# Optimization experiments

Hardware: AMD Instinct MI355X
Metric: run time of the kernel (lower is better)

The kernel has to match this reference:

```python
import jax, jax.numpy as jnp
import numpy as np

N = 100000
E = 2000000
F = 64          # in_features == out_features (required by attention * h_j)
BETA = 0.5
NEG_SLOPE = 0.01  # torch F.leaky_relu default


def setup_inputs() -> dict:
    key = jax.random.key(0)
    k1, k2, k3, k4, k5, k6 = jax.random.split(key, 6)
    h = jax.random.normal(k1, (N, F), dtype=jnp.float32)
    adj = jax.random.randint(k2, (2, E), 0, N, dtype=jnp.int64)
    amount = jax.random.uniform(k3, (E,), dtype=jnp.float32)
    count = jax.random.uniform(k4, (E,), dtype=jnp.float32)
    fc_w = jax.random.normal(k5, (F, 2 * F), dtype=jnp.float32) * (1.0 / np.sqrt(2 * F))
    fc_b = jax.random.normal(k6, (F,), dtype=jnp.float32) * 0.01
    return {"h": h, "adj": adj, "amount": amount, "count": count,
            "fc_w": fc_w, "fc_b": fc_b}


def _minmax_norm(x):
    lo, hi = x.min(), x.max()
    return (x - lo) / (hi - lo + 1e-8)


def reference(h, adj, amount, count, fc_w, fc_b):
    # per-edge weight from normalized amount/count
    edge_weight = BETA * _minmax_norm(amount) + (1.0 - BETA) * _minmax_norm(count)  # [E]

    src, dst = adj[0], adj[1]
    h_i = h[src]                     # [E, F]
    h_j = h[dst]                     # [E, F]
    h_cat = jnp.concatenate([h_i, h_j], axis=1)  # [E, 2F]

    score = jnp.einsum('ef,of->eo', h_cat, fc_w) + fc_b  # [E, F_out]
    score = jnp.where(score >= 0, score, NEG_SLOPE * score)  # leaky_relu
    score = score * edge_weight[:, None]

    # softmax over ALL edges (dim 0), per feature, as in the original
    attention = jax.nn.softmax(score, axis=0)  # [E, F]

    agg = jnp.zeros_like(h).at[src].add(attention * h_j)  # scatter-add -> [N, F]
    return agg
```

## Files before the change

kernel.cpp:

```cpp
#include <hip/hip_runtime.h>
#include <hip/hip_fp16.h>
#include <math.h>

#define FDIM   64
#define NB     16
#define BSHIFT 7
#define BMASK  127
#define EPTA   16
#define CHUNKA (EPTA * 256)
#define SCH    1024
#define DMASK  0xFFFFF

__global__ __launch_bounds__(256) void count_mm_k(const int* __restrict__ src,
                                                  const float* __restrict__ amount,
                                                  const float* __restrict__ count,
                                                  int* __restrict__ mat,
                                                  float4* __restrict__ partial,
                                                  double* __restrict__ colsum,
                                                  int E, int nblkA, int nbkt) {
  __shared__ int lhist[1024];
  __shared__ float4 lred[4];
  for (int k = threadIdx.x; k < nbkt; k += 256) lhist[k] = 0;
  if (blockIdx.x == 0)
    for (int i = threadIdx.x; i < 1024; i += 256) colsum[i] = 0.0;
  __syncthreads();
  float amin = 3.4e38f, amax = -3.4e38f, cmin = 3.4e38f, cmax = -3.4e38f;
  int e0 = blockIdx.x * CHUNKA + threadIdx.x * EPTA;
  if (e0 + EPTA <= E) {
    #pragma unroll
    for (int q = 0; q < EPTA; q += 4) {
      int4   s4 = *(const int4*)(src + e0 + q);
      float4 a4 = *(const float4*)(amount + e0 + q);
      float4 c4 = *(const float4*)(count + e0 + q);
      atomicAdd(&lhist[s4.x >> BSHIFT], 1);
      atomicAdd(&lhist[s4.y >> BSHIFT], 1);
      atomicAdd(&lhist[s4.z >> BSHIFT], 1);
      atomicAdd(&lhist[s4.w >> BSHIFT], 1);
      amin = fminf(amin, fminf(fminf(a4.x, a4.y), fminf(a4.z, a4.w)));
      amax = fmaxf(amax, fmaxf(fmaxf(a4.x, a4.y), fmaxf(a4.z, a4.w)));
      cmin = fminf(cmin, fminf(fminf(c4.x, c4.y), fminf(c4.z, c4.w)));
      cmax = fmaxf(cmax, fmaxf(fmaxf(c4.x, c4.y), fmaxf(c4.z, c4.w)));
    }
  } else {
    for (int e = e0; e < E; e++) {
      atomicAdd(&lhist[src[e] >> BSHIFT], 1);
      float a = amount[e], c = count[e];
      amin = fminf(amin, a); amax = fmaxf(amax, a);
      cmin = fminf(cmin, c); cmax = fmaxf(cmax, c);
    }
  }
  #pragma unroll
  for (int off = 32; off; off >>= 1) {
    amin = fminf(amin, __shfl_down(amin, off));
    amax = fmaxf(amax, __shfl_down(amax, off));
    cmin = fminf(cmin, __shfl_down(cmin, off));
    cmax = fmaxf(cmax, __shfl_down(cmax, off));
  }
  if ((threadIdx.x & 63) == 0) lred[threadIdx.x >> 6] = make_float4(amin, amax, cmin, cmax);
  __syncthreads();
  for (int k = threadIdx.x; k < nbkt; k += 256)
    mat[(size_t)k * nblkA + blockIdx.x] = lhist[k];
  if (threadIdx.x == 0) {
    float4 r = lred[0];
    #pragma unroll
    for (int w = 1; w < 4; w++) {
      r.x = fminf(r.x, lred[w].x); r.y = fmaxf(r.y, lred[w].y);
      r.z = fminf(r.z, lred[w].z); r.w = fmaxf(r.w, lred[w].w);
    }
    partial[blockIdx.x] = r;
  }
}

__global__ __launch_bounds__(256) void scan1_k(const int* __restrict__ v,
                                               int* __restrict__ bsum, int M) {
  __shared__ int lds[256];
  int t = threadIdx.x, b = blockIdx.x;
  int s = 0;
  for (int i = b * SCH + t; i < min((b + 1) * SCH, M); i += 256) s += v[i];
  lds[t] = s; __syncthreads();
  for (int off = 128; off; off >>= 1) {
    if (t < off) lds[t] += lds[t + off];
    __syncthreads();
  }
  if (t == 0) bsum[b] = lds[0];
}

__global__ __launch_bounds__(256) void scan2_k(const int* __restrict__ bsum,
                                               int* __restrict__ bexcl, int nchunk,
                                               const float4* __restrict__ partial,
                                               float* __restrict__ mmf, int nb) {
  __shared__ int lds[256];
  int t = threadIdx.x;
  int running = 0;
  for (int c0 = 0; c0 < nchunk; c0 += 256) {
    int x = (c0 + t < nchunk) ? bsum[c0 + t] : 0;
    lds[t] = x; __syncthreads();
    for (int off = 1; off < 256; off <<= 1) {
      int v = (t >= off) ? lds[t - off] : 0;
      __syncthreads();
      lds[t] += v; __syncthreads();
    }
    if (c0 + t < nchunk) bexcl[c0 + t] = running + lds[t] - x;
    running += lds[255];
    __syncthreads();
  }
  float amin = 3.4e38f, amax = -3.4e38f, cmin = 3.4e38f, cmax = -3.4e38f;
  for (int i = t; i < nb; i += 256) {
    float4 p = partial[i];
    amin = fminf(amin, p.x); amax = fmaxf(amax, p.y);
    cmin = fminf(cmin, p.z); cmax = fmaxf(cmax, p.w);
  }
  #pragma unroll
  for (int off = 32; off; off >>= 1) {
    amin = fminf(amin, __shfl_down(amin, off));
    amax = fmaxf(amax, __shfl_down(amax, off));
    cmin = fminf(cmin, __shfl_down(cmin, off));
    cmax = fmaxf(cmax, __shfl_down(cmax, off));
  }
  __shared__ float4 lred[4];
  if ((t & 63) == 0) lred[t >> 6] = make_float4(amin, amax, cmin, cmax);
  __syncthreads();
  if (t == 0) {
    float4 r = lred[0];
    #pragma unroll
    for (int w = 1; w < 4; w++) {
      r.x = fminf(r.x, lred[w].x); r.y = fmaxf(r.y, lred[w].y);
      r.z = fminf(r.z, lred[w].z); r.w = fmaxf(r.w, lred[w].w);
    }
    mmf[0] = r.x; mmf[1] = r.y; mmf[2] = r.z; mmf[3] = r.w;
  }
}

__global__ __launch_bounds__(256) void scan3_k(const int* __restrict__ v,
                                               const int* __restrict__ bexcl,
                                               int* __restrict__ smat, int M) {
  __shared__ int lds[256];
  int t = threadIdx.x, b = blockIdx.x;
  int running = bexcl[b];
  for (int tile = 0; tile < SCH; tile += 256) {
    int i = b * SCH + tile + t;
    int x = (i < M) ? v[i] : 0;
    lds[t] = x; __syncthreads();
    for (int off = 1; off < 256; off <<= 1) {
      int vv = (t >= off) ? lds[t - off] : 0;
      __syncthreads();
      lds[t] += vv; __syncthreads();
    }
    if (i < M) smat[i] = running + lds[t] - x;
    running += lds[255];
    __syncthreads();
  }
}

__global__ __launch_bounds__(256) void scatter_k(const int* __restrict__ src,
                                                 const int* __restrict__ dst,
                                                 const float* __restrict__ amount,
                                                 const float* __restrict__ count,
                                                 const float* __restrict__ mmf,
                                                 const int* __restrict__ smat,
                                                 int2* __restrict__ payload,
                                                 int E, int nblkA, int nbkt) {
  __shared__ int cntb[1024];
  __shared__ int baseb[1024];
  __shared__ int sbase[1024];
  __shared__ int tmp[256];
  __shared__ int2 lpay[CHUNKA];
  __shared__ int lgpos[CHUNKA];
  const int t = threadIdx.x, blk = blockIdx.x;
  for (int k = t; k < nbkt; k += 256) {
    cntb[k] = 0;
    sbase[k] = smat[(size_t)k * nblkA + blk];
  }
  __syncthreads();
  const float amin = mmf[0], amax = mmf[1], cmin = mmf[2], cmax = mmf[3];
  const float L2E = 1.4426950408889634f;
  const float ascale = 0.5f * L2E / (amax - amin + 1e-8f);
  const float cscale = 0.5f * L2E / (cmax - cmin + 1e-8f);
  int e0 = blk * CHUNKA + t * EPTA;
  const bool full = (e0 + EPTA <= E);
  int4 S[4]; int4 D[4]; float4 A[4]; float4 C[4];
  if (full) {
    #pragma unroll
    for (int q = 0; q < 4; q++) {
      S[q] = *(const int4*)(src + e0 + 4 * q);
      D[q] = *(const int4*)(dst + e0 + 4 * q);
      A[q] = *(const float4*)(amount + e0 + 4 * q);
      C[q] = *(const float4*)(count + e0 + 4 * q);
      atomicAdd(&cntb[S[q].x >> BSHIFT], 1);
      atomicAdd(&cntb[S[q].y >> BSHIFT], 1);
      atomicAdd(&cntb[S[q].z >> BSHIFT], 1);
      atomicAdd(&cntb[S[q].w >> BSHIFT], 1);
    }
  } else {
    for (int e = e0; e < E; e++) atomicAdd(&cntb[src[e] >> BSHIFT], 1);
  }
  __syncthreads();
  int running = 0;
  for (int c0 = 0; c0 < nbkt; c0 += 256) {
    int x = (c0 + t < nbkt) ? cntb[c0 + t] : 0;
    tmp[t] = x; __syncthreads();
    for (int off = 1; off < 256; off <<= 1) {
      int v = (t >= off) ? tmp[t - off] : 0;
      __syncthreads();
      tmp[t] += v; __syncthreads();
    }
    if (c0 + t < nbkt) baseb[c0 + t] = running + tmp[t] - x;
    running += tmp[255];
    __syncthreads();
  }
  for (int k = t; k < nbkt; k += 256) cntb[k] = baseb[k];
  __syncthreads();
  auto ins = [&](int s, int d, float a, float c) {
    int b = s >> BSHIFT;
    float ew = (a - amin) * ascale + (c - cmin) * cscale;
    int pos = atomicAdd(&cntb[b], 1);
    lpay[pos] = make_int2(d | ((s & BMASK) << 20), __float_as_int(ew));
    lgpos[pos] = sbase[b] + (pos - baseb[b]);
  };
  if (full) {
    #pragma unroll
    for (int q = 0; q < 4; q++) {
      ins(S[q].x, D[q].x, A[q].x, C[q].x);
      ins(S[q].y, D[q].y, A[q].y, C[q].y);
      ins(S[q].z, D[q].z, A[q].z, C[q].z);
      ins(S[q].w, D[q].w, A[q].w, C[q].w);
    }
  } else {
    for (int e = e0; e < E; e++) ins(src[e], dst[e], amount[e], count[e]);
  }
  __syncthreads();
  const int ned = min(CHUNKA, E - blk * CHUNKA);
  for (int i = t; i < ned; i += 256) payload[lgpos[i]] = lpay[i];
}

__global__ __launch_bounds__(256) void binB_k(const int2* __restrict__ payload,
                                              const int* __restrict__ smat,
                                              int* __restrict__ hist,
                                              int* __restrict__ offsets,
                                              int2* __restrict__ edge_s,
                                              int E, int nblkA, int nbkt, int N) {
  __shared__ int fcnt[128];
  __shared__ int fs[128];
  __shared__ int fcur[128];
  const int b = blockIdx.x;
  const int t = threadIdx.x;
  const int base = smat[(size_t)b * nblkA];
  const int end  = (b + 1 < nbkt) ? smat[(size_t)(b + 1) * nblkA] : E;
  if (t < 128) fcnt[t] = 0;
  __syncthreads();
  for (int i = base + t; i < end; i += 256)
    atomicAdd(&fcnt[payload[i].x >> 20], 1);
  __syncthreads();
  if (t < 128) fs[t] = fcnt[t];
  __syncthreads();
  for (int off = 1; off < 128; off <<= 1) {
    int v = 0;
    if (t < 128 && t >= off) v = fs[t - off];
    __syncthreads();
    if (t < 128) fs[t] += v;
    __syncthreads();
  }
  if (t < 128) {
    int excl = fs[t] - fcnt[t];
    fcur[t] = base + excl;
    int node = (b << BSHIFT) + t;
    if (node < N) { hist[node] = fcnt[t]; offsets[node] = base + excl; }
  }
  __syncthreads();
  for (int i = base + t; i < end; i += 256) {
    int2 v = payload[i];
    int pos = atomicAdd(&fcur[v.x >> 20], 1);
    edge_s[pos] = make_int2(v.x & DMASK, v.y);
  }
}

__global__ __launch_bounds__(128) void pre_gemm(const float* __restrict__ h,
                                                const float* __restrict__ fc_w,
                                                const float* __restrict__ fc_b,
                                                float* __restrict__ G1,
                                                __half2* __restrict__ P, int N) {
  __shared__ float hs[NB * FDIM];
  const int t = threadIdx.x;
  const int o = t & 63, half = t >> 6;
  float w[FDIM];
  const float* wrow = fc_w + o * 128 + half * 64;
  #pragma unroll
  for (int f = 0; f < FDIM; f += 4) {
    float4 v = *(const float4*)(wrow + f);
    w[f] = v.x; w[f + 1] = v.y; w[f + 2] = v.z; w[f + 3] = v.w;
  }
  const float bias = (half == 0) ? fc_b[o] : 0.0f;
  const int n0 = blockIdx.x * NB;
  const int nrows = min(NB, N - n0);
  for (int i = t; i < nrows * FDIM; i += 128) hs[i] = h[(size_t)n0 * FDIM + i];
  __syncthreads();
  for (int n = 0; n < nrows; n++) {
    float acc = bias;
    #pragma unroll
    for (int f = 0; f < FDIM; f += 4) {
      float4 hv = *(const float4*)(&hs[n * FDIM + f]);
      acc += hv.x * w[f] + hv.y * w[f + 1] + hv.z * w[f + 2] + hv.w * w[f + 3];
    }
    if (half == 0) {
      G1[(size_t)(n0 + n) * FDIM + o] = acc;
    } else {
      P[(size_t)(n0 + n) * FDIM + o] =
          __halves2half2(__float2half(acc), __float2half(hs[n * FDIM + o]));
    }
  }
}

__device__ __forceinline__ float2 unpack_h2(unsigned u) {
  __half2 v = *(__half2*)&u;
  return make_float2(__low2float(v), __high2float(v));
}

__global__ __launch_bounds__(256) void fused_k(const int* __restrict__ offsets,
                                               const int* __restrict__ hist,
                                               const int2* __restrict__ edge_s,
                                               const float* __restrict__ G1,
                                               const unsigned* __restrict__ P,
                                               double* __restrict__ colsum,
                                               float* __restrict__ out, int N) {
  const int lane = threadIdx.x & 63;
  const int wid = blockIdx.x * 4 + (threadIdx.x >> 6);
  const int nw = gridDim.x * 4;
  float csum = 0.0f;
  for (int n = wid; n < N; n += nw) {
    float g1 = G1[(size_t)n * FDIM + lane];
    float acc = 0.0f;
    int start = offsets[n], cnt = hist[n];
    for (int j0 = 0; j0 < cnt; j0 += 64) {
      int m = min(64, cnt - j0);
      int2 p = make_int2(0, 0);
      if (lane < m) p = edge_s[start + j0 + lane];
      int j = 0;
      for (; j + 16 <= m; j += 16) {
        int dd[16]; float ee[16]; unsigned uu[16];
        #pragma unroll
        for (int k = 0; k < 16; k++) {
          dd[k] = __builtin_amdgcn_readlane(p.x, j + k);
          ee[k] = __int_as_float(__builtin_amdgcn_readlane(p.y, j + k));
        }
        #pragma unroll
        for (int k = 0; k < 16; k++) uu[k] = P[(size_t)dd[k] * FDIM + lane];
        #pragma unroll
        for (int k = 0; k < 16; k++) {
          float2 v = unpack_h2(uu[k]);
          float sc = g1 + v.x;
          sc = fmaxf(sc, 0.01f * sc);
          float x = exp2f(sc * ee[k]);
          csum += x;
          acc += x * v.y;
        }
      }
      for (; j < m; j += 8) {
        int rem = m - j;
        int dd[8]; float ee[8], wm[8]; unsigned uu[8];
        #pragma unroll
        for (int k = 0; k < 8; k++) {
          dd[k] = __builtin_amdgcn_readlane(p.x, j + k);
          ee[k] = __int_as_float(__builtin_amdgcn_readlane(p.y, j + k));
          wm[k] = (k < rem) ? 1.0f : 0.0f;
        }
        #pragma unroll
        for (int k = 0; k < 8; k++) uu[k] = P[(size_t)dd[k] * FDIM + lane];
        #pragma unroll
        for (int k = 0; k < 8; k++) {
          float2 v = unpack_h2(uu[k]);
          float sc = g1 + v.x;
          sc = fmaxf(sc, 0.01f * sc);
          float x = exp2f(sc * ee[k]) * wm[k];
          csum += x;
          acc += x * v.y;
        }
      }
    }
    out[(size_t)n * FDIM + lane] = acc;
  }
  __shared__ float part[256];
  part[threadIdx.x] = csum;
  __syncthreads();
  if (threadIdx.x < 64) {
    float tot = part[threadIdx.x] + part[threadIdx.x + 64] +
                part[threadIdx.x + 128] + part[threadIdx.x + 192];
    atomicAdd(&colsum[threadIdx.x * 16], (double)tot);
  }
}

__global__ __launch_bounds__(256) void scale_k(float4* __restrict__ out4,
                                               const double* __restrict__ colsum,
                                               int total4) {
  __shared__ float rinv_s[64];
  if (threadIdx.x < 64) rinv_s[threadIdx.x] = (float)(1.0 / colsum[threadIdx.x * 16]);
  __syncthreads();
  const float4* r4 = (const float4*)rinv_s;
  int idx = blockIdx.x * blockDim.x + threadIdx.x;
  int stride = gridDim.x * blockDim.x;
  for (int i = idx; i < total4; i += stride) {
    float4 v = out4[i];
    float4 r = r4[i & 15];
    v.x *= r.x; v.y *= r.y; v.z *= r.z; v.w *= r.w;
    out4[i] = v;
  }
}

extern "C" void kernel_launch(void* const* d_in, const int* in_sizes, int n_in,
                              void* d_out, int out_size, void* d_ws, size_t ws_size,
                              hipStream_t stream) {
  const float* h      = (const float*)d_in[0];
  const int*   adj    = (const int*)d_in[1];
  const float* amount = (const float*)d_in[2];
  const float* count  = (const float*)d_in[3];
  const float* fc_w   = (const float*)d_in[4];
  const float* fc_b   = (const float*)d_in[5];
  float* out = (float*)d_out;

  const int E = in_sizes[2];
  const int N = in_sizes[0] / FDIM;
  const int* src = adj;
  const int* dst = adj + E;
  const int nbkt  = (N + BMASK) >> BSHIFT;
  const int nblkA = (E + CHUNKA - 1) / CHUNKA;
  const int M = nbkt * nblkA;
  const int nchunk = (M + SCH - 1) / SCH;

  char* ws = (char*)d_ws;
  size_t off = 0;
  auto alloc = [&](size_t bytes) { void* p = ws + off; off += (bytes + 255) & ~(size_t)255; return p; };
  float*    G1      = (float*)alloc((size_t)N * FDIM * sizeof(float));
  __half2*  P       = (__half2*)alloc((size_t)N * FDIM * sizeof(__half2));
  int2*     edge_s  = (int2*)alloc((size_t)E * sizeof(int2));
  int2*     payload = (int2*)alloc((size_t)E * sizeof(int2));
  int*      hist    = (int*)alloc((size_t)N * sizeof(int));
  int*      offsets = (int*)alloc((size_t)N * sizeof(int));
  int*      mat     = (int*)alloc((size_t)M * sizeof(int));
  int*      smat    = (int*)alloc((size_t)M * sizeof(int));
  int*      bsum    = (int*)alloc((size_t)nchunk * sizeof(int));
  int*      bexcl   = (int*)alloc((size_t)nchunk * sizeof(int));
  float4*   mmpart  = (float4*)alloc((size_t)nblkA * sizeof(float4));
  double*   colsum  = (double*)alloc(1024 * sizeof(double));
  float*    mmf     = (float*)alloc(4 * sizeof(float));

  count_mm_k<<<nblkA, 256, 0, stream>>>(src, amount, count, mat, mmpart, colsum, E, nblkA, nbkt);
  scan1_k<<<nchunk, 256, 0, stream>>>(mat, bsum, M);
  scan2_k<<<1, 256, 0, stream>>>(bsum, bexcl, nchunk, mmpart, mmf, nblkA);
  scan3_k<<<nchunk, 256, 0, stream>>>(mat, bexcl, smat, M);
  scatter_k<<<nblkA, 256, 0, stream>>>(src, dst, amount, count, mmf, smat, payload, E, nblkA, nbkt);
  binB_k<<<nbkt, 256, 0, stream>>>(payload, smat, hist, offsets, edge_s, E, nblkA, nbkt, N);
  pre_gemm<<<(N + NB - 1) / NB, 128, 0, stream>>>(h, fc_w, fc_b, G1, P, N);
  fused_k<<<4096, 256, 0, stream>>>(offsets, hist, edge_s, G1, (const unsigned*)P, colsum, out, N);
  scale_k<<<1024, 256, 0, stream>>>((float4*)out, colsum, N * FDIM / 4);
}
```

Before: 306.8 us.

## Balance fused kernel by edge ranges with segmented node accumulation and atomic flushes

The fused aggregation kernel now gives each wave an equal, 64-aligned slice of the sorted edge list instead of a fixed set of nodes. Node identity is rebuilt from the bucket boundaries (binary search on smat) plus the in-bucket index kept in the payload. Partial sums for nodes cut at slice boundaries are combined with atomicAdd into an output that is zeroed first, while interior nodes are written directly. The scatter kernel's block scan now uses wave shuffles instead of LDS barrier loops, and the per-node hist/offsets arrays are dropped. The aim is to remove load imbalance and the extra metadata traffic, at the cost of a memset, per-edge node-change checks and some atomics.

```diff
diff --git a/kernel.cpp b/kernel.cpp
--- a/kernel.cpp
+++ b/kernel.cpp
@@ -163,7 +163,7 @@
   __shared__ int cntb[1024];
   __shared__ int baseb[1024];
   __shared__ int sbase[1024];
-  __shared__ int tmp[256];
+  __shared__ int wsum[4];
   __shared__ int2 lpay[CHUNKA];
   __shared__ int lgpos[CHUNKA];
   const int t = threadIdx.x, blk = blockIdx.x;
@@ -195,19 +195,39 @@
     for (int e = e0; e < E; e++) atomicAdd(&cntb[src[e] >> BSHIFT], 1);
   }
   __syncthreads();
-  int running = 0;
-  for (int c0 = 0; c0 < nbkt; c0 += 256) {
-    int x = (c0 + t < nbkt) ? cntb[c0 + t] : 0;
-    tmp[t] = x; __syncthreads();
-    for (int off = 1; off < 256; off <<= 1) {
-      int v = (t >= off) ? tmp[t - off] : 0;
-      __syncthreads();
-      tmp[t] += v; __syncthreads();
-    }
-    if (c0 + t < nbkt) baseb[c0 + t] = running + tmp[t] - x;
-    running += tmp[255];
-    __syncthreads();
-  }
+  {
+    const int wv = t >> 6, ln = t & 63;
+    int carry = 0;
+    #pragma unroll
+    for (int c = 0; c < 4; c++) {
+      int idx = (wv << 8) + (c << 6) + ln;
+      int x = (idx < nbkt) ? cntb[idx] : 0;
+      int v = x;
+      #pragma unroll
+      for (int off = 1; off < 64; off <<= 1) {
+        int u = __shfl_up(v, off);
+        if (ln >= off) v += u;
+      }
+      if (idx < nbkt) baseb[idx] = carry + v - x;
+      carry += __shfl(v, 63);
+    }
+    if (ln == 0) wsum[wv] = carry;
+  }
+  __syncthreads();
+  {
+    const int wv = t >> 6, ln = t & 63;
+    int wpre = 0;
+    #pragma unroll
+    for (int i = 0; i < 4; i++) wpre += (i < wv) ? wsum[i] : 0;
+    if (wpre) {
+      #pragma unroll
+      for (int c = 0; c < 4; c++) {
+        int idx = (wv << 8) + (c << 6) + ln;
+        if (idx < nbkt) baseb[idx] += wpre;
+      }
+    }
+  }
+  __syncthreads();
   for (int k = t; k < nbkt; k += 256) cntb[k] = baseb[k];
   __syncthreads();
   auto ins = [&](int s, int d, float a, float c) {
@@ -235,10 +255,8 @@
 
 __global__ __launch_bounds__(256) void binB_k(const int2* __restrict__ payload,
                                               const int* __restrict__ smat,
-                                              int* __restrict__ hist,
-                                              int* __restrict__ offsets,
                                               int2* __restrict__ edge_s,
-                                              int E, int nblkA, int nbkt, int N) {
+                                              int E, int nblkA, int nbkt) {
   __shared__ int fcnt[128];
   __shared__ int fs[128];
   __shared__ int fcur[128];
@@ -260,17 +278,12 @@
     if (t < 128) fs[t] += v;
     __syncthreads();
   }
-  if (t < 128) {
-    int excl = fs[t] - fcnt[t];
-    fcur[t] = base + excl;
-    int node = (b << BSHIFT) + t;
-    if (node < N) { hist[node] = fcnt[t]; offsets[node] = base + excl; }
-  }
+  if (t < 128) fcur[t] = base + fs[t] - fcnt[t];
   __syncthreads();
   for (int i = base + t; i < end; i += 256) {
     int2 v = payload[i];
     int pos = atomicAdd(&fcur[v.x >> 20], 1);
-    edge_s[pos] = make_int2(v.x & DMASK, v.y);
+    edge_s[pos] = v;
   }
 }
 
@@ -315,68 +328,104 @@
   return make_float2(__low2float(v), __high2float(v));
 }
 
-__global__ __launch_bounds__(256) void fused_k(const int* __restrict__ offsets,
-                                               const int* __restrict__ hist,
-                                               const int2* __restrict__ edge_s,
+__global__ __launch_bounds__(256) void fused_k(const int2* __restrict__ edge_s,
+                                               const int* __restrict__ smat,
                                                const float* __restrict__ G1,
                                                const unsigned* __restrict__ P,
                                                double* __restrict__ colsum,
-                                               float* __restrict__ out, int N) {
+                                               float* __restrict__ out,
+                                               int E, int nblkA, int nbkt) {
   const int lane = threadIdx.x & 63;
-  const int wid = blockIdx.x * 4 + (threadIdx.x >> 6);
+  const int wv = __builtin_amdgcn_readfirstlane(threadIdx.x >> 6);
+  const int wid = blockIdx.x * 4 + wv;
   const int nw = gridDim.x * 4;
   float csum = 0.0f;
-  for (int n = wid; n < N; n += nw) {
-    float g1 = G1[(size_t)n * FDIM + lane];
-    float acc = 0.0f;
-    int start = offsets[n], cnt = hist[n];
-    for (int j0 = 0; j0 < cnt; j0 += 64) {
-      int m = min(64, cnt - j0);
+  const int per = (((E + nw - 1) / nw) + 63) & ~63;
+  const int e0 = wid * per;
+  const int e1 = min(e0 + per, E);
+  if (e0 < E) {
+    int lo = 0, hi = nbkt - 1;
+    while (lo < hi) {
+      int mid = (lo + hi + 1) >> 1;
+      if (smat[(size_t)mid * nblkA] <= e0) lo = mid; else hi = mid - 1;
+    }
+    int bkt = lo;
+    int nextb = (bkt + 1 < nbkt) ? smat[(size_t)(bkt + 1) * nblkA] : E;
+    int curnode = -1;
+    bool firstf = true;
+    float acc = 0.0f, g1 = 0.0f;
+    auto flush_to = [&](int node) {
+      if (curnode >= 0) {
+        float* dp = out + (size_t)curnode * FDIM + lane;
+        if (firstf) { atomicAdd(dp, acc); firstf = false; }
+        else *dp = acc;
+      }
+      curnode = node; acc = 0.0f;
+      g1 = G1[(size_t)node * FDIM + lane];
+    };
+    for (int c0 = e0; c0 < e1; c0 += 64) {
+      const int m = min(64, e1 - c0);
       int2 p = make_int2(0, 0);
-      if (lane < m) p = edge_s[start + j0 + lane];
-      int j = 0;
-      for (; j + 16 <= m; j += 16) {
-        int dd[16]; float ee[16]; unsigned uu[16];
-        #pragma unroll
-        for (int k = 0; k < 16; k++) {
-          dd[k] = __builtin_amdgcn_readlane(p.x, j + k);
-          ee[k] = __int_as_float(__builtin_amdgcn_readlane(p.y, j + k));
+      if (lane < m) p = edge_s[c0 + lane];
+      if (m == 64) {
+        #pragma unroll 1
+        for (int j = 0; j < 64; j += 16) {
+          int dd[16], nd[16]; float ee[16]; unsigned uu[16];
+          #pragma unroll
+          for (int k = 0; k < 16; k++) {
+            int x = __builtin_amdgcn_readlane(p.x, j + k);
+            ee[k] = __int_as_float(__builtin_amdgcn_readlane(p.y, j + k));
+            dd[k] = x & DMASK;
+            nd[k] = x >> 20;
+          }
+          #pragma unroll
+          for (int k = 0; k < 16; k++) uu[k] = P[(size_t)dd[k] * FDIM + lane];
+          #pragma unroll
+          for (int k = 0; k < 16; k++) {
+            int i = c0 + j + k;
+            while (i >= nextb) { bkt++; nextb = (bkt + 1 < nbkt) ? smat[(size_t)(bkt + 1) * nblkA] : E; }
+            int node = (bkt << BSHIFT) + nd[k];
+            if (node != curnode) flush_to(node);
+            float2 v = unpack_h2(uu[k]);
+            float sc = g1 + v.x;
+            sc = fmaxf(sc, 0.01f * sc);
+            float x = exp2f(sc * ee[k]);
+            csum += x;
+            acc += x * v.y;
+          }
         }
-        #pragma unroll
-        for (int k = 0; k < 16; k++) uu[k] = P[(size_t)dd[k] * FDIM + lane];
-        #pragma unroll
-        for (int k = 0; k < 16; k++) {
-          float2 v = unpack_h2(uu[k]);
-          float sc = g1 + v.x;
-          sc = fmaxf(sc, 0.01f * sc);
-          float x = exp2f(sc * ee[k]);
-          csum += x;
-          acc += x * v.y;
+      } else {
+        for (int j = 0; j < m; j += 16) {
+          const int rem = m - j;
+          int dd[16], nd[16]; float ee[16]; unsigned uu[16];
+          #pragma unroll
+          for (int k = 0; k < 16; k++) {
+            int x = __builtin_amdgcn_readlane(p.x, j + k);
+            ee[k] = __int_as_float(__builtin_amdgcn_readlane(p.y, j + k));
+            dd[k] = x & DMASK;
+            nd[k] = x >> 20;
+          }
+          #pragma unroll
+          for (int k = 0; k < 16; k++) uu[k] = P[(size_t)dd[k] * FDIM + lane];
+          #pragma unroll
+          for (int k = 0; k < 16; k++) {
+            if (k < rem) {
+              int i = c0 + j + k;
+              while (i >= nextb) { bkt++; nextb = (bkt + 1 < nbkt) ? smat[(size_t)(bkt + 1) * nblkA] : E; }
+              int node = (bkt << BSHIFT) + nd[k];
+              if (node != curnode) flush_to(node);
+              float2 v = unpack_h2(uu[k]);
+              float sc = g1 + v.x;
+              sc = fmaxf(sc, 0.01f * sc);
+              float x = exp2f(sc * ee[k]);
+              csum += x;
+              acc += x * v.y;
+            }
+          }
         }
       }
-      for (; j < m; j += 8) {
-        int rem = m - j;
-        int dd[8]; float ee[8], wm[8]; unsigned uu[8];
-        #pragma unroll
-        for (int k = 0; k < 8; k++) {
-          dd[k] = __builtin_amdgcn_readlane(p.x, j + k);
-          ee[k] = __int_as_float(__builtin_amdgcn_readlane(p.y, j + k));
-          wm[k] = (k < rem) ? 1.0f : 0.0f;
-        }
-        #pragma unroll
-        for (int k = 0; k < 8; k++) uu[k] = P[(size_t)dd[k] * FDIM + lane];
-        #pragma unroll
-        for (int k = 0; k < 8; k++) {
-          float2 v = unpack_h2(uu[k]);
-          float sc = g1 + v.x;
-          sc = fmaxf(sc, 0.01f * sc);
-          float x = exp2f(sc * ee[k]) * wm[k];
-          csum += x;
-          acc += x * v.y;
-        }
-      }
-    }
-    out[(size_t)n * FDIM + lane] = acc;
+    }
+    if (curnode >= 0) atomicAdd(out + (size_t)curnode * FDIM + lane, acc);
   }
   __shared__ float part[256];
   part[threadIdx.x] = csum;
@@ -432,8 +481,6 @@
   __half2*  P       = (__half2*)alloc((size_t)N * FDIM * sizeof(__half2));
   int2*     edge_s  = (int2*)alloc((size_t)E * sizeof(int2));
   int2*     payload = (int2*)alloc((size_t)E * sizeof(int2));
-  int*      hist    = (int*)alloc((size_t)N * sizeof(int));
-  int*      offsets = (int*)alloc((size_t)N * sizeof(int));
   int*      mat     = (int*)alloc((size_t)M * sizeof(int));
   int*      smat    = (int*)alloc((size_t)M * sizeof(int));
   int*      bsum    = (int*)alloc((size_t)nchunk * sizeof(int));
@@ -442,13 +489,14 @@
   double*   colsum  = (double*)alloc(1024 * sizeof(double));
   float*    mmf     = (float*)alloc(4 * sizeof(float));
 
+  hipMemsetAsync(d_out, 0, (size_t)out_size * sizeof(float), stream);
   count_mm_k<<<nblkA, 256, 0, stream>>>(src, amount, count, mat, mmpart, colsum, E, nblkA, nbkt);
   scan1_k<<<nchunk, 256, 0, stream>>>(mat, bsum, M);
   scan2_k<<<1, 256, 0, stream>>>(bsum, bexcl, nchunk, mmpart, mmf, nblkA);
   scan3_k<<<nchunk, 256, 0, stream>>>(mat, bexcl, smat, M);
   scatter_k<<<nblkA, 256, 0, stream>>>(src, dst, amount, count, mmf, smat, payload, E, nblkA, nbkt);
-  binB_k<<<nbkt, 256, 0, stream>>>(payload, smat, hist, offsets, edge_s, E, nblkA, nbkt, N);
+  binB_k<<<nbkt, 256, 0, stream>>>(payload, smat, edge_s, E, nblkA, nbkt);
   pre_gemm<<<(N + NB - 1) / NB, 128, 0, stream>>>(h, fc_w, fc_b, G1, P, N);
-  fused_k<<<4096, 256, 0, stream>>>(offsets, hist, edge_s, G1, (const unsigned*)P, colsum, out, N);
+  fused_k<<<4096, 256, 0, stream>>>(edge_s, smat, G1, (const unsigned*)P, colsum, out, E, nblkA, nbkt);
   scale_k<<<1024, 256, 0, stream>>>((float4*)out, colsum, N * FDIM / 4);
 }
```

Result: no change. 302.7 us (-1.3%).
